# Optimization experiments

Measured on AMD Instinct MI355X. Metric: run time of the kernel, lower is better.

Reference implementation:

```python
import jax, jax.numpy as jnp
import numpy as np

ALPHA = 0.2  # Config.alpha, GAT default LeakyReLU slope
NUM_REL = 4
N = 4096          # num_e == batch of nodes
IN_F = 256
OUT_F = 64


def setup_inputs() -> dict:
    key = jax.random.key(0)
    k1, k2, k3, k4 = jax.random.split(key, 4)
    inp = jax.random.normal(k1, (N, IN_F), dtype=jnp.float32)
    adj = jax.random.uniform(k2, (N, N), dtype=jnp.float32)
    # xavier_uniform with gain=1.414 (sqrt(2))
    gain = 1.414
    limW = gain * np.sqrt(6.0 / (IN_F + OUT_F))
    W = jax.random.uniform(k3, (IN_F, OUT_F), minval=-limW, maxval=limW, dtype=jnp.float32)
    lima = gain * np.sqrt(6.0 / (2 * OUT_F + 1))
    a = jax.random.uniform(k4, (2 * OUT_F, 1), minval=-lima, maxval=lima, dtype=jnp.float32)
    return {"input": inp, "adj": adj, "W": W, "a": a}


def reference(input, adj, W, a):
    # h: (N, F_out)
    h = input @ W
    # The torch code builds an (N, N, 2F) concat tensor then matmuls with a.
    # Algebraically: e_ij = leakyrelu(h_i . a1 + h_j . a2) with a = [a1; a2].
    a1, a2 = a[:OUT_F], a[OUT_F:]            # (F,1) each
    s1 = (h @ a1)                            # (N,1) -> row term
    s2 = (h @ a2)                            # (N,1) -> col term
    e = jax.nn.leaky_relu(s1 + s2.T, negative_slope=ALPHA)  # (N,N)
    # attention = adj * e, replicated per relation, softmax over keys (dim 2)
    att = adj * e                            # (N,N)
    att = jnp.broadcast_to(att[None, :, :], (NUM_REL, N, N))
    att = jax.nn.softmax(att, axis=2)        # (R,N,N)
    # dropout is identity in eval mode
    h_prime = jnp.einsum('rij,jf->rif', att, h)  # (R,N,F_out)
    return jax.nn.elu(h_prime)               # concat=True -> elu
```

## Files before the change

kernel.cpp:

```cpp
#include <hip/hip_runtime.h>


#define NN 4096
#define INF 256
#define OUTF 64
#define ALPHA 0.2f

typedef __bf16 bf16;
typedef __bf16 bf16x8 __attribute__((ext_vector_type(8)));
typedef float floatx4 __attribute__((ext_vector_type(4)));

__global__ __launch_bounds__(256) void k_h(const float* __restrict__ input,
                                           const float* __restrict__ W,
                                           const float* __restrict__ a,
                                           bf16* __restrict__ hT,
                                           float* __restrict__ s1,
                                           float* __restrict__ s2) {
    const int wid  = threadIdx.x >> 6;
    const int lane = threadIdx.x & 63;
    const int row  = blockIdx.x * 4 + wid;
    const float* in_row = input + (size_t)row * INF;
    float acc = 0.f;
    #pragma unroll 8
    for (int k = 0; k < INF; ++k)
        acc = fmaf(in_row[k], W[k * OUTF + lane], acc);
    hT[(size_t)lane * NN + row] = (bf16)acc;
    float v1 = acc * a[lane];
    float v2 = acc * a[OUTF + lane];
    #pragma unroll
    for (int off = 32; off; off >>= 1) {
        v1 += __shfl_down(v1, off);
        v2 += __shfl_down(v2, off);
    }
    if (lane == 0) { s1[row] = v1; s2[row] = v2; }
}

__global__ __launch_bounds__(512, 1) void k_f(const float* __restrict__ adj,
                                              const float* __restrict__ s1,
                                              const float* __restrict__ s2,
                                              const bf16* __restrict__ hT,
                                              float* __restrict__ out) {
    const int b    = blockIdx.x;
    const int tid  = threadIdx.x;
    const int w    = tid >> 6;
    const int lane = tid & 63;
    const int q = lane >> 4, r = lane & 15;
    const int i = b * 16 + r;

    const float s1i = s1[i];
    const float* arow = adj + (size_t)i * NN;

    floatx4 acc[4] = {{0,0,0,0},{0,0,0,0},{0,0,0,0},{0,0,0,0}};
    float lsum = 0.f;
    const int jw = w * 512;

    #pragma unroll 4
    for (int t = 0; t < 16; ++t) {
        const int jb = jw + t * 32 + q * 8;
        const float4 a0  = *(const float4*)(arow + jb);
        const float4 a1  = *(const float4*)(arow + jb + 4);
        const float4 sv0 = *(const float4*)(s2 + jb);
        const float4 sv1 = *(const float4*)(s2 + jb + 4);
        float p0, p1, p2, p3, p4, p5, p6, p7, e;
        e = s1i + sv0.x; e = (e > 0.f ? e : ALPHA * e) * a0.x; p0 = __expf(e);
        e = s1i + sv0.y; e = (e > 0.f ? e : ALPHA * e) * a0.y; p1 = __expf(e);
        e = s1i + sv0.z; e = (e > 0.f ? e : ALPHA * e) * a0.z; p2 = __expf(e);
        e = s1i + sv0.w; e = (e > 0.f ? e : ALPHA * e) * a0.w; p3 = __expf(e);
        e = s1i + sv1.x; e = (e > 0.f ? e : ALPHA * e) * a1.x; p4 = __expf(e);
        e = s1i + sv1.y; e = (e > 0.f ? e : ALPHA * e) * a1.y; p5 = __expf(e);
        e = s1i + sv1.z; e = (e > 0.f ? e : ALPHA * e) * a1.z; p6 = __expf(e);
        e = s1i + sv1.w; e = (e > 0.f ? e : ALPHA * e) * a1.w; p7 = __expf(e);
        lsum += ((p0 + p1) + (p2 + p3)) + ((p4 + p5) + (p6 + p7));
        bf16x8 af;
        af[0] = (bf16)p0; af[1] = (bf16)p1; af[2] = (bf16)p2; af[3] = (bf16)p3;
        af[4] = (bf16)p4; af[5] = (bf16)p5; af[6] = (bf16)p6; af[7] = (bf16)p7;
        #pragma unroll
        for (int nt = 0; nt < 4; ++nt) {
            const bf16x8 bf = *(const bf16x8*)(hT + (size_t)(nt * 16 + r) * NN + jb);
            acc[nt] = __builtin_amdgcn_mfma_f32_16x16x32_bf16(af, bf, acc[nt], 0, 0, 0);
        }
    }

    lsum += __shfl_xor(lsum, 16);
    lsum += __shfl_xor(lsum, 32);

    __shared__ float sacc[8][1024];
    __shared__ float slr[8][16];
    #pragma unroll
    for (int nt = 0; nt < 4; ++nt)
        #pragma unroll
        for (int reg = 0; reg < 4; ++reg)
            sacc[w][(q * 4 + reg) * 64 + nt * 16 + r] = acc[nt][reg];
    if (q == 0) slr[w][r] = lsum;
    __syncthreads();

    #pragma unroll
    for (int k = 0; k < 2; ++k) {
        const int idx = tid + k * 512;
        const int row = idx >> 6, f = idx & 63;
        float s = 0.f, l = 0.f;
        #pragma unroll
        for (int ww = 0; ww < 8; ++ww) { s += sacc[ww][idx]; l += slr[ww][row]; }
        float v = s / l;
        v = v > 0.f ? v : (__expf(v) - 1.f);
        const size_t o = (size_t)(b * 16 + row) * OUTF + f;
        #pragma unroll
        for (int rr = 0; rr < 4; ++rr) out[(size_t)rr * (NN * OUTF) + o] = v;
    }
}

extern "C" void kernel_launch(void* const* d_in, const int* in_sizes, int n_in,
                              void* d_out, int out_size, void* d_ws, size_t ws_size,
                              hipStream_t stream) {
    (void)in_sizes; (void)n_in; (void)out_size; (void)ws_size;
    const float* input = (const float*)d_in[0];
    const float* adj   = (const float*)d_in[1];
    const float* W     = (const float*)d_in[2];
    const float* a     = (const float*)d_in[3];
    float* out = (float*)d_out;

    char* ws = (char*)d_ws;
    bf16*  hT = (bf16*)ws;
    float* s1 = (float*)(ws + (512 << 10));
    float* s2 = (float*)(ws + (528 << 10));

    hipLaunchKernelGGL(k_h, dim3(NN / 4), dim3(256), 0, stream, input, W, a, hT, s1, s2);
    hipLaunchKernelGGL(k_f, dim3(NN / 16), dim3(512), 0, stream, adj, s1, s2, hT, out);
}
```

Before: 136.0 us.

## Stage adj tiles into LDS via async global_load_lds double buffering

After: 136.6 us. About the same (+0.5%).

```diff
diff --git a/kernel.cpp b/kernel.cpp
--- a/kernel.cpp
+++ b/kernel.cpp
@@ -5,10 +5,17 @@
 #define INF 256
 #define OUTF 64
 #define ALPHA 0.2f
+#define JTILE 256
+#define NTILES (NN / JTILE)
+#define TPAD 260
 
 typedef __bf16 bf16;
 typedef __bf16 bf16x8 __attribute__((ext_vector_type(8)));
 typedef float floatx4 __attribute__((ext_vector_type(4)));
+
+typedef const __attribute__((address_space(1))) void GV;
+typedef __attribute__((address_space(3))) void LV;
+#define GLD16(g, l) __builtin_amdgcn_global_load_lds((GV*)(g), (LV*)(l), 16, 0, 0)
 
 __global__ __launch_bounds__(256) void k_h(const float* __restrict__ input,
                                            const float* __restrict__ W,
@@ -40,25 +47,39 @@
                                               const float* __restrict__ s2,
                                               const bf16* __restrict__ hT,
                                               float* __restrict__ out) {
+    __shared__ __align__(16) float tile[2][16 * TPAD];
+    __shared__ float sacc[8][1024];
+    __shared__ float slr[8][16];
+
     const int b    = blockIdx.x;
     const int tid  = threadIdx.x;
     const int w    = tid >> 6;
     const int lane = tid & 63;
     const int q = lane >> 4, r = lane & 15;
-    const int i = b * 16 + r;
-
-    const float s1i = s1[i];
-    const float* arow = adj + (size_t)i * NN;
+    const int i0 = b * 16;
+    const float s1i = s1[i0 + r];
 
     floatx4 acc[4] = {{0,0,0,0},{0,0,0,0},{0,0,0,0},{0,0,0,0}};
     float lsum = 0.f;
-    const int jw = w * 512;
 
-    #pragma unroll 4
-    for (int t = 0; t < 16; ++t) {
-        const int jb = jw + t * 32 + q * 8;
-        const float4 a0  = *(const float4*)(arow + jb);
-        const float4 a1  = *(const float4*)(arow + jb + 4);
+    #define STAGE(buf, t)                                                              \
+        do {                                                                           \
+            const float* g0 = adj + (size_t)(i0 + w) * NN + (t) * JTILE + lane * 4;    \
+            const float* g1 = adj + (size_t)(i0 + w + 8) * NN + (t) * JTILE + lane * 4;\
+            GLD16(g0, &tile[buf][w * TPAD]);                                           \
+            GLD16(g1, &tile[buf][(w + 8) * TPAD]);                                     \
+        } while (0)
+
+    STAGE(0, 0);
+    for (int t = 0; t < NTILES; ++t) {
+        const int buf = t & 1;
+        __syncthreads();
+        if (t + 1 < NTILES) STAGE(buf ^ 1, t + 1);
+
+        const int jb = t * JTILE + w * 32 + q * 8;
+        const float* ap = &tile[buf][r * TPAD + w * 32 + q * 8];
+        const float4 a0  = *(const float4*)ap;
+        const float4 a1  = *(const float4*)(ap + 4);
         const float4 sv0 = *(const float4*)(s2 + jb);
         const float4 sv1 = *(const float4*)(s2 + jb + 4);
         float p0, p1, p2, p3, p4, p5, p6, p7, e;
@@ -80,12 +101,11 @@
             acc[nt] = __builtin_amdgcn_mfma_f32_16x16x32_bf16(af, bf, acc[nt], 0, 0, 0);
         }
     }
+    #undef STAGE
 
     lsum += __shfl_xor(lsum, 16);
     lsum += __shfl_xor(lsum, 32);
 
-    __shared__ float sacc[8][1024];
-    __shared__ float slr[8][16];
     #pragma unroll
     for (int nt = 0; nt < 4; ++nt)
         #pragma unroll
@@ -103,7 +123,7 @@
         for (int ww = 0; ww < 8; ++ww) { s += sacc[ww][idx]; l += slr[ww][row]; }
         float v = s / l;
         v = v > 0.f ? v : (__expf(v) - 1.f);
-        const size_t o = (size_t)(b * 16 + row) * OUTF + f;
+        const size_t o = (size_t)(i0 + row) * OUTF + f;
         #pragma unroll
         for (int rr = 0; rr < 4; ++rr) out[(size_t)rr * (NN * OUTF) + o] = v;
     }
```
